# Kernel tuning notes

Hardware: AMD Instinct MI355X
Metric: run time of the kernel (lower is better)

Reference implementation:

```python
import jax, jax.numpy as jnp
import numpy as np

D_MODEL = 768
NUM_HEADS = 12
D_K = D_MODEL // NUM_HEADS


def setup_inputs() -> dict:
    key = jax.random.key(0)
    ks = jax.random.split(key, 9)
    B, S = 2, 4096
    x = jax.random.normal(ks[0], (B, S, D_MODEL), dtype=jnp.float32)
    s = 1.0 / np.sqrt(D_MODEL)
    Wq = jax.random.normal(ks[1], (D_MODEL, D_MODEL), dtype=jnp.float32) * s
    Wk = jax.random.normal(ks[2], (D_MODEL, D_MODEL), dtype=jnp.float32) * s
    Wv = jax.random.normal(ks[3], (D_MODEL, D_MODEL), dtype=jnp.float32) * s
    Wo = jax.random.normal(ks[4], (D_MODEL, D_MODEL), dtype=jnp.float32) * s
    bq = jnp.zeros((D_MODEL,), dtype=jnp.float32)
    bk = jnp.zeros((D_MODEL,), dtype=jnp.float32)
    bv = jnp.zeros((D_MODEL,), dtype=jnp.float32)
    bo = jnp.zeros((D_MODEL,), dtype=jnp.float32)
    return {"x": x, "Wq": Wq, "bq": bq, "Wk": Wk, "bk": bk,
            "Wv": Wv, "bv": bv, "Wo": Wo, "bo": bo}


def _split_heads(t):
    B, S, _ = t.shape
    return t.reshape(B, S, NUM_HEADS, D_K).transpose(0, 2, 1, 3)  # [B,H,S,d_k]


def reference(x, Wq, bq, Wk, bk, Wv, bv, Wo, bo):
    Q = _split_heads(x @ Wq.T + bq)
    K = _split_heads(x @ Wk.T + bk)
    V = _split_heads(x @ Wv.T + bv)
    scale = 1.0 / jnp.sqrt(jnp.float32(D_K))
    scores = jnp.einsum('bhqd,bhkd->bhqk', Q, K) * scale  # [B,H,S,S]
    attn = jax.nn.softmax(scores, axis=-1)
    out = jnp.einsum('bhqk,bhkd->bhqd', attn, V)          # [B,H,S,d_k]
    B, _, S, _ = out.shape
    out = out.transpose(0, 2, 1, 3).reshape(B, S, D_MODEL)
    return out @ Wo.T + bo
```

## Files before the change

kernel.cpp:

```cpp
#include <hip/hip_runtime.h>
#include <hip/hip_bf16.h>
#include <stdint.h>

typedef __hip_bfloat16 bf16;
typedef __attribute__((ext_vector_type(8))) short short8;
typedef __attribute__((ext_vector_type(4))) float f32x4;
typedef __attribute__((ext_vector_type(16))) float f32x16;

#define MFMA16(a, b, c) __builtin_amdgcn_mfma_f32_16x16x32_bf16((a), (b), (c), 0, 0, 0)
#define MFMA32(a, b, c) __builtin_amdgcn_mfma_f32_32x32x16_bf16((a), (b), (c), 0, 0, 0)

__device__ __forceinline__ unsigned short f2bf(float f) {
  bf16 h = __float2bfloat16(f);
  unsigned short u;
  __builtin_memcpy(&u, &h, 2);
  return u;
}

__device__ __forceinline__ uint32_t cvtpk(float lo, float hi) {
  uint32_t r;
  asm("v_cvt_pk_bf16_f32 %0, %1, %2" : "=v"(r) : "v"(lo), "v"(hi));
  return r;
}

__device__ __forceinline__ void pl32swap(uint32_t& a, uint32_t& b) {
  asm volatile("v_permlane32_swap_b32 %0, %1" : "+v"(a), "+v"(b));
}

__device__ __forceinline__ void gload_lds16(const void* g, void* l) {
  __builtin_amdgcn_global_load_lds(
      (const __attribute__((address_space(1))) uint32_t*)g,
      (__attribute__((address_space(3))) uint32_t*)l, 16, 0, 0);
}

__device__ __forceinline__ int swz_chunk(int row, int c) { return c ^ (row & 7); }

__global__ __launch_bounds__(256) void cvt_all(
    const float* __restrict__ x,
    const float* __restrict__ w0, const float* __restrict__ w1,
    const float* __restrict__ w2, const float* __restrict__ w3,
    bf16* __restrict__ xo,
    bf16* __restrict__ o0, bf16* __restrict__ o1,
    bf16* __restrict__ o2, bf16* __restrict__ o3) {
  int idx = blockIdx.x * 256 + threadIdx.x;
  const float* src;
  bf16* dst;
  int i;
  if (idx < 1572864) {
    src = x; dst = xo; i = idx;
  } else {
    int r = idx - 1572864;
    int w = r / 147456;
    i = r - w * 147456;
    src = (w == 0) ? w0 : (w == 1) ? w1 : (w == 2) ? w2 : w3;
    dst = (w == 0) ? o0 : (w == 1) ? o1 : (w == 2) ? o2 : o3;
  }
  float4 v = ((const float4*)src)[i];
  ushort4 u;
  u.x = f2bf(v.x); u.y = f2bf(v.y); u.z = f2bf(v.z); u.w = f2bf(v.w);
  ((ushort4*)dst)[i] = u;
}

__global__ __launch_bounds__(256, 4) void gemm_qkv(
    const bf16* __restrict__ A,
    const bf16* __restrict__ Wqb, const bf16* __restrict__ Wkb,
    const bf16* __restrict__ Wvb,
    const float* __restrict__ bq, const float* __restrict__ bk,
    const float* __restrict__ bv,
    bf16* __restrict__ Qh, bf16* __restrict__ Kh, bf16* __restrict__ Vh,
    float sq) {
  __shared__ bf16 As[128 * 64];
  __shared__ bf16 Bs[128 * 64];
  const int tid = threadIdx.x;
  const int lane = tid & 63, wid = tid >> 6;
  const int wr = wid >> 1, wc = wid & 1;
  const int l15 = lane & 15, lhi = lane >> 4;
  const int tm = blockIdx.x * 128;
  const int by = blockIdx.y;
  const int seg = by / 6;
  const int tn = (by - seg * 6) * 128;

  const bf16* B = (seg == 0) ? Wqb : (seg == 1) ? Wkb : Wvb;
  const float* bias = (seg == 0) ? bq : (seg == 1) ? bk : bv;
  bf16* dst = (seg == 0) ? Qh : (seg == 1) ? Kh : Vh;
  const float scale = (seg == 0) ? sq : 1.0f;
  const int K = 768;

  f32x4 zero = {0.f, 0.f, 0.f, 0.f};
  f32x4 acc[4][4];
  for (int i = 0; i < 4; ++i)
    for (int j = 0; j < 4; ++j) acc[i][j] = zero;

  for (int k0 = 0; k0 < K; k0 += 64) {
    __syncthreads();
    for (int it = 0; it < 4; ++it) {
      int o = (tid + it * 256) << 4;
      int row = o >> 7, c = (o >> 4) & 7;
      int sw = swz_chunk(row, c) << 4;
      gload_lds16((const char*)A + (((size_t)(tm + row) * K + k0) << 1) + sw, (char*)As + o);
      gload_lds16((const char*)B + (((size_t)(tn + row) * K + k0) << 1) + sw, (char*)Bs + o);
    }
    __syncthreads();
    for (int ks = 0; ks < 2; ++ks) {
      short8 af[4], bfr[4];
      for (int mi = 0; mi < 4; ++mi) {
        int row = wr * 64 + mi * 16 + l15;
        af[mi] = *(const short8*)((const char*)As + row * 128 +
                                  (swz_chunk(row, ks * 4 + lhi) << 4));
      }
      for (int ni = 0; ni < 4; ++ni) {
        int row = wc * 64 + ni * 16 + l15;
        bfr[ni] = *(const short8*)((const char*)Bs + row * 128 +
                                   (swz_chunk(row, ks * 4 + lhi) << 4));
      }
      for (int mi = 0; mi < 4; ++mi)
        for (int ni = 0; ni < 4; ++ni)
          acc[mi][ni] = MFMA16(af[mi], bfr[ni], acc[mi][ni]);
    }
  }

  for (int mi = 0; mi < 4; ++mi)
    for (int ni = 0; ni < 4; ++ni)
      for (int j = 0; j < 4; ++j) {
        int m = tm + wr * 64 + mi * 16 + lhi * 4 + j;
        int n = tn + wc * 64 + ni * 16 + l15;
        float v = (acc[mi][ni][j] + bias[n]) * scale;
        int b = m >> 12, s = m & 4095, h = n >> 6, d = n & 63;
        dst[(((size_t)(b * 12 + h) * 4096 + s) << 6) + d] = __float2bfloat16(v);
      }
}

__global__ __launch_bounds__(256, 4) void gemm_wo(
    const bf16* __restrict__ A, const bf16* __restrict__ B,
    const float* __restrict__ bias, float* __restrict__ C) {
  __shared__ bf16 As[128 * 64];
  __shared__ bf16 Bs[64 * 64];
  const int tid = threadIdx.x;
  const int lane = tid & 63, wid = tid >> 6;
  const int l15 = lane & 15, lhi = lane >> 4;
  const int tm = blockIdx.x * 128, tn = blockIdx.y * 64;
  const int K = 768;

  f32x4 zero = {0.f, 0.f, 0.f, 0.f};
  f32x4 acc[2][4];
  for (int i = 0; i < 2; ++i)
    for (int j = 0; j < 4; ++j) acc[i][j] = zero;

  for (int k0 = 0; k0 < K; k0 += 64) {
    __syncthreads();
    for (int it = 0; it < 4; ++it) {
      int o = (tid + it * 256) << 4;
      int row = o >> 7, c = (o >> 4) & 7;
      int sw = swz_chunk(row, c) << 4;
      gload_lds16((const char*)A + (((size_t)(tm + row) * K + k0) << 1) + sw, (char*)As + o);
    }
    for (int it = 0; it < 2; ++it) {
      int o = (tid + it * 256) << 4;
      int row = o >> 7, c = (o >> 4) & 7;
      int sw = swz_chunk(row, c) << 4;
      gload_lds16((const char*)B + (((size_t)(tn + row) * K + k0) << 1) + sw, (char*)Bs + o);
    }
    __syncthreads();
    for (int ks = 0; ks < 2; ++ks) {
      short8 af[2], bfr[4];
      for (int mi = 0; mi < 2; ++mi) {
        int row = wid * 32 + mi * 16 + l15;
        af[mi] = *(const short8*)((const char*)As + row * 128 +
                                  (swz_chunk(row, ks * 4 + lhi) << 4));
      }
      for (int ni = 0; ni < 4; ++ni) {
        int row = ni * 16 + l15;
        bfr[ni] = *(const short8*)((const char*)Bs + row * 128 +
                                   (swz_chunk(row, ks * 4 + lhi) << 4));
      }
      for (int mi = 0; mi < 2; ++mi)
        for (int ni = 0; ni < 4; ++ni)
          acc[mi][ni] = MFMA16(af[mi], bfr[ni], acc[mi][ni]);
    }
  }

  for (int mi = 0; mi < 2; ++mi)
    for (int ni = 0; ni < 4; ++ni)
      for (int j = 0; j < 4; ++j) {
        int m = tm + wid * 32 + mi * 16 + lhi * 4 + j;
        int n = tn + ni * 16 + l15;
        C[(size_t)m * 768 + n] = acc[mi][ni][j] + bias[n];
      }
}

__global__ __launch_bounds__(256) void transpose_v(const bf16* __restrict__ Vh,
                                                   bf16* __restrict__ VTh) {
  __shared__ bf16 T[64 * 64];
  const int tid = threadIdx.x;
  const int bh = blockIdx.x >> 6;
  const int t = blockIdx.x & 63;
  const char* src = (const char*)(Vh + ((size_t)bh * 4096 + t * 64) * 64);
  char* dst = (char*)(VTh + ((size_t)bh * 64) * 4096 + t * 64);

  for (int it = 0; it < 2; ++it) {
    int idx = tid + it * 256;
    int r = idx & 63, cc = idx >> 6;
    uint4 vv = *(const uint4*)(src + r * 128 + cc * 16);
    unsigned short sv[8];
    __builtin_memcpy(sv, &vv, 16);
#pragma unroll
    for (int jj = 0; jj < 8; ++jj) {
      int d = cc * 8 + jj;
      *(unsigned short*)((char*)T + d * 128 + (swz_chunk(d, r >> 3) << 4) +
                         ((r & 7) << 1)) = sv[jj];
    }
  }
  __syncthreads();
  for (int it = 0; it < 2; ++it) {
    int idx = tid + it * 256;
    int d = idx >> 3, c = idx & 7;
    uint4 vv = *(const uint4*)((const char*)T + d * 128 + (swz_chunk(d, c) << 4));
    *(uint4*)(dst + (size_t)d * 8192 + c * 16) = vv;
  }
}

__global__ __launch_bounds__(256, 3) void attn_kernel(
    const bf16* __restrict__ Qh, const bf16* __restrict__ Kh,
    const bf16* __restrict__ VTh, bf16* __restrict__ AO) {
  __shared__ float4 smem4[34816 / 16];
  char* smraw = (char*)smem4;
#define KT(b) (smraw + (b) * 8192)
#define VT(b) (smraw + 16384 + (b) * 8192)
  float* OX = (float*)smraw;

  const int tid = threadIdx.x;
  const int lane = tid & 63, wid = tid >> 6;
  const int l31 = lane & 31, h = lane >> 5;
  const int qsub = wid & 1, kvh = wid >> 1;

  const int bh = blockIdx.x >> 5;
  const int qt = blockIdx.x & 31;

  const size_t hb = (size_t)bh * 4096 * 64;
  const bf16* Qb = Qh + hb;
  const bf16* Kb = Kh + hb;
  const char* Vg0 = (const char*)(VTh + hb);
  const int qb = qt * 128 + qsub * 64;

  short8 qf[2][4];
#pragma unroll
  for (int j = 0; j < 2; ++j)
#pragma unroll
    for (int ki = 0; ki < 4; ++ki)
      qf[j][ki] = *(const short8*)((const char*)Qb + (size_t)(qb + 32 * j + l31) * 128 +
                                   ki * 32 + h * 16);

  f32x16 z16;
  for (int i = 0; i < 16; ++i) z16[i] = 0.f;
  f32x16 o00 = z16, o01 = z16, o10 = z16, o11 = z16;
  float psum0 = 0.f, psum1 = 0.f;

  const int krow = kvh * 32 + l31;

  for (int it = 0; it < 2; ++it) {
    int o = (tid + it * 256) << 4;
    int row = o >> 7, c = (o >> 4) & 7;
    int sw = swz_chunk(row, c) << 4;
    gload_lds16((const char*)Kb + row * 128 + sw, KT(0) + o);
    gload_lds16(Vg0 + row * 8192 + sw, VT(0) + o);
  }
  __syncthreads();

  int cur = 0;
  for (int kt = 0; kt < 64; ++kt) {
    if (kt < 63) {
      const char* Kg = (const char*)(Kb + (size_t)(kt + 1) * 4096);
      const char* Vg = Vg0 + (size_t)(kt + 1) * 128;
      char* Kd = KT(cur ^ 1);
      char* Vd = VT(cur ^ 1);
      for (int it = 0; it < 2; ++it) {
        int o = (tid + it * 256) << 4;
        int row = o >> 7, c = (o >> 4) & 7;
        int sw = swz_chunk(row, c) << 4;
        gload_lds16(Kg + row * 128 + sw, Kd + o);
        gload_lds16(Vg + row * 8192 + sw, Vd + o);
      }
    }

    const char* Kl = KT(cur);
    const char* Vl = VT(cur);

    f32x16 s0, s1;
    __builtin_amdgcn_s_setprio(1);
    {
      short8 kf = *(const short8*)(Kl + krow * 128 + (swz_chunk(krow, h) << 4));
      s0 = MFMA32(kf, qf[0][0], z16);
      s1 = MFMA32(kf, qf[1][0], z16);
    }
#pragma unroll
    for (int ki = 1; ki < 4; ++ki) {
      short8 kf = *(const short8*)(Kl + krow * 128 + (swz_chunk(krow, 2 * ki + h) << 4));
      s0 = MFMA32(kf, qf[0][ki], s0);
      s1 = MFMA32(kf, qf[1][ki], s1);
    }
    __builtin_amdgcn_s_setprio(0);

    short8 pb[2][2];
#pragma unroll
    for (int j = 0; j < 2; ++j) {
#pragma unroll
      for (int kk = 0; kk < 2; ++kk) {
        float p[8];
#pragma unroll
        for (int e = 0; e < 8; ++e)
          p[e] = __builtin_amdgcn_exp2f(j ? s1[8 * kk + e] : s0[8 * kk + e]);
        float ps = ((p[0] + p[1]) + (p[2] + p[3])) + ((p[4] + p[5]) + (p[6] + p[7]));
        if (j) psum1 += ps; else psum0 += ps;
        uint32_t A0 = cvtpk(p[0], p[1]), A1 = cvtpk(p[2], p[3]);
        uint32_t B0 = cvtpk(p[4], p[5]), B1 = cvtpk(p[6], p[7]);
        pl32swap(A0, B0);
        pl32swap(A1, B1);
        uint32_t w[4] = {A0, A1, B0, B1};
        short8 frag;
        __builtin_memcpy(&frag, w, 16);
        pb[j][kk] = frag;
      }
    }

    __builtin_amdgcn_s_setprio(1);
#pragma unroll
    for (int kk = 0; kk < 2; ++kk) {
      short8 v0 = *(const short8*)(Vl + l31 * 128 +
                                   (swz_chunk(l31, 4 * kvh + 2 * kk + h) << 4));
      short8 v1 = *(const short8*)(Vl + (32 + l31) * 128 +
                                   (swz_chunk(32 + l31, 4 * kvh + 2 * kk + h) << 4));
      o00 = MFMA32(v0, pb[0][kk], o00);
      o01 = MFMA32(v0, pb[1][kk], o01);
      o10 = MFMA32(v1, pb[0][kk], o10);
      o11 = MFMA32(v1, pb[1][kk], o11);
    }
    __builtin_amdgcn_s_setprio(0);

    __syncthreads();
    cur ^= 1;
  }

  psum0 += __shfl_xor(psum0, 32);
  psum1 += __shfl_xor(psum1, 32);

  float* W = OX + (size_t)(qsub * 64 + lane) * 68;
  if (kvh == 1) {
#pragma unroll
    for (int g = 0; g < 4; ++g) {
      *(float4*)(W + 0 * 16 + 4 * g) = make_float4(o00[4*g], o00[4*g+1], o00[4*g+2], o00[4*g+3]);
      *(float4*)(W + 1 * 16 + 4 * g) = make_float4(o01[4*g], o01[4*g+1], o01[4*g+2], o01[4*g+3]);
      *(float4*)(W + 2 * 16 + 4 * g) = make_float4(o10[4*g], o10[4*g+1], o10[4*g+2], o10[4*g+3]);
      *(float4*)(W + 3 * 16 + 4 * g) = make_float4(o11[4*g], o11[4*g+1], o11[4*g+2], o11[4*g+3]);
    }
    W[64] = psum0;
    W[65] = psum1;
  }
  __syncthreads();
  if (kvh == 0) {
#pragma unroll
    for (int g = 0; g < 4; ++g) {
      float4 a0 = *(const float4*)(W + 0 * 16 + 4 * g);
      float4 a1 = *(const float4*)(W + 1 * 16 + 4 * g);
      float4 a2 = *(const float4*)(W + 2 * 16 + 4 * g);
      float4 a3 = *(const float4*)(W + 3 * 16 + 4 * g);
      o00[4*g] += a0.x; o00[4*g+1] += a0.y; o00[4*g+2] += a0.z; o00[4*g+3] += a0.w;
      o01[4*g] += a1.x; o01[4*g+1] += a1.y; o01[4*g+2] += a1.z; o01[4*g+3] += a1.w;
      o10[4*g] += a2.x; o10[4*g+1] += a2.y; o10[4*g+2] += a2.z; o10[4*g+3] += a2.w;
      o11[4*g] += a3.x; o11[4*g+1] += a3.y; o11[4*g+2] += a3.z; o11[4*g+3] += a3.w;
    }
    psum0 += W[64];
    psum1 += W[65];
    float pinv0 = 1.0f / psum0;
    float pinv1 = 1.0f / psum1;

    const int b = bh / 12, hd = bh % 12;
#pragma unroll
    for (int j = 0; j < 2; ++j) {
      int q = qb + 32 * j + l31;
      char* base = (char*)AO + (((size_t)(b * 4096 + q)) * 768 + hd * 64) * 2;
      float pv = j ? pinv1 : pinv0;
#pragma unroll
      for (int t = 0; t < 2; ++t) {
#pragma unroll
        for (int u = 0; u < 4; ++u) {
          ushort4 us;
          float v0 = (t ? (j ? o11[4*u+0] : o10[4*u+0]) : (j ? o01[4*u+0] : o00[4*u+0]));
          float v1 = (t ? (j ? o11[4*u+1] : o10[4*u+1]) : (j ? o01[4*u+1] : o00[4*u+1]));
          float v2 = (t ? (j ? o11[4*u+2] : o10[4*u+2]) : (j ? o01[4*u+2] : o00[4*u+2]));
          float v3 = (t ? (j ? o11[4*u+3] : o10[4*u+3]) : (j ? o01[4*u+3] : o00[4*u+3]));
          us.x = f2bf(v0 * pv);
          us.y = f2bf(v1 * pv);
          us.z = f2bf(v2 * pv);
          us.w = f2bf(v3 * pv);
          int d0 = 32 * t + 8 * u + 4 * h;
          *(ushort4*)(base + d0 * 2) = us;
        }
      }
    }
  }
#undef KT
#undef VT
}

extern "C" void kernel_launch(void* const* d_in, const int* in_sizes, int n_in,
                              void* d_out, int out_size, void* d_ws, size_t ws_size,
                              hipStream_t stream) {
  (void)in_sizes; (void)n_in; (void)out_size; (void)ws_size;
  const float* x  = (const float*)d_in[0];
  const float* Wq = (const float*)d_in[1];
  const float* bq = (const float*)d_in[2];
  const float* Wk = (const float*)d_in[3];
  const float* bk = (const float*)d_in[4];
  const float* Wv = (const float*)d_in[5];
  const float* bv = (const float*)d_in[6];
  const float* Wo = (const float*)d_in[7];
  const float* bo = (const float*)d_in[8];

  char* ws = (char*)d_ws;
  bf16* Qh  = (bf16*)(ws + 0);
  bf16* Kh  = (bf16*)(ws + 12582912);
  bf16* Vh  = (bf16*)(ws + 25165824);
  bf16* xb  = (bf16*)(ws + 37748736);
  bf16* Wqb = (bf16*)(ws + 50331648);
  bf16* Wkb = (bf16*)(ws + 51511296);
  bf16* Wvb = (bf16*)(ws + 52690944);
  bf16* Wob = (bf16*)(ws + 53870592);
  bf16* VTh = xb;
  bf16* AO  = Vh;

  cvt_all<<<8448, 256, 0, stream>>>(x, Wq, Wk, Wv, Wo, xb, Wqb, Wkb, Wvb, Wob);

  const float SQ = 0.125f * 1.4426950408889634f;
  dim3 gq(64, 18);
  gemm_qkv<<<gq, 256, 0, stream>>>(xb, Wqb, Wkb, Wvb, bq, bk, bv,
                                   Qh, Kh, Vh, SQ);
  transpose_v<<<1536, 256, 0, stream>>>(Vh, VTh);
  attn_kernel<<<768, 256, 0, stream>>>(Qh, Kh, VTh, AO);
  dim3 gw(64, 12);
  gemm_wo<<<gw, 256, 0, stream>>>(AO, Wob, bo, (float*)d_out);
}
```

Baseline: 189.0 us.

## Software-pipeline attention loop: overlap next QK with previous PV, triple-buffer V

Restructures the attention main loop so each iteration computes QK^T for tile kt, then PV for tile kt-1 using probabilities from the prior iteration, then the exp for tile kt. This lets the MFMA work of the two matmuls interleave with the exp/convert work instead of running in strict dependency order. V gets a third LDS buffer, growing shared memory from about 34KB to 40KB, which may hurt occupancy at 3 blocks per CU. The V transpose kernel is also changed to pack two rows into 32-bit LDS writes with a simpler XOR swizzle, cutting LDS store count.

```diff
diff --git a/kernel.cpp b/kernel.cpp
--- a/kernel.cpp
+++ b/kernel.cpp
@@ -197,18 +197,17 @@
   const char* src = (const char*)(Vh + ((size_t)bh * 4096 + t * 64) * 64);
   char* dst = (char*)(VTh + ((size_t)bh * 64) * 4096 + t * 64);
 
-  for (int it = 0; it < 2; ++it) {
-    int idx = tid + it * 256;
-    int r = idx & 63, cc = idx >> 6;
-    uint4 vv = *(const uint4*)(src + r * 128 + cc * 16);
-    unsigned short sv[8];
-    __builtin_memcpy(sv, &vv, 16);
-#pragma unroll
-    for (int jj = 0; jj < 8; ++jj) {
-      int d = cc * 8 + jj;
-      *(unsigned short*)((char*)T + d * 128 + (swz_chunk(d, r >> 3) << 4) +
-                         ((r & 7) << 1)) = sv[jj];
-    }
+  const int rp = tid & 31, cc = tid >> 5;
+  uint4 va = *(const uint4*)(src + (2 * rp) * 128 + cc * 16);
+  uint4 vb = *(const uint4*)(src + (2 * rp + 1) * 128 + cc * 16);
+  unsigned short a16[8], b16[8];
+  __builtin_memcpy(a16, &va, 16);
+  __builtin_memcpy(b16, &vb, 16);
+#pragma unroll
+  for (int jj = 0; jj < 8; ++jj) {
+    uint32_t w = (uint32_t)a16[jj] | ((uint32_t)b16[jj] << 16);
+    *(uint32_t*)((char*)T + (cc * 8 + jj) * 128 + (((rp >> 2) ^ jj) << 4) +
+                 ((rp & 3) << 2)) = w;
   }
   __syncthreads();
   for (int it = 0; it < 2; ++it) {
@@ -222,10 +221,10 @@
 __global__ __launch_bounds__(256, 3) void attn_kernel(
     const bf16* __restrict__ Qh, const bf16* __restrict__ Kh,
     const bf16* __restrict__ VTh, bf16* __restrict__ AO) {
-  __shared__ float4 smem4[34816 / 16];
+  __shared__ float4 smem4[40960 / 16];
   char* smraw = (char*)smem4;
-#define KT(b) (smraw + (b) * 8192)
-#define VT(b) (smraw + 16384 + (b) * 8192)
+#define KTB(b) (smraw + (b) * 8192)
+#define VTB(b) (smraw + 16384 + (b) * 8192)
   float* OX = (float*)smraw;
 
   const int tid = threadIdx.x;
@@ -257,88 +256,99 @@
 
   const int krow = kvh * 32 + l31;
 
-  for (int it = 0; it < 2; ++it) {
-    int o = (tid + it * 256) << 4;
-    int row = o >> 7, c = (o >> 4) & 7;
-    int sw = swz_chunk(row, c) << 4;
-    gload_lds16((const char*)Kb + row * 128 + sw, KT(0) + o);
-    gload_lds16(Vg0 + row * 8192 + sw, VT(0) + o);
-  }
+#define STAGE_K(gbase, dstb)                                             \
+  for (int it = 0; it < 2; ++it) {                                       \
+    int o = (tid + it * 256) << 4;                                       \
+    int row = o >> 7, c = (o >> 4) & 7;                                  \
+    gload_lds16((gbase) + row * 128 + (swz_chunk(row, c) << 4), (dstb) + o); \
+  }
+#define STAGE_V(gbase, dstb)                                             \
+  for (int it = 0; it < 2; ++it) {                                       \
+    int o = (tid + it * 256) << 4;                                       \
+    int row = o >> 7, c = (o >> 4) & 7;                                  \
+    gload_lds16((gbase) + row * 8192 + (swz_chunk(row, c) << 4), (dstb) + o); \
+  }
+
+#define DO_QK(Kl)                                                        \
+  {                                                                      \
+    short8 kf = *(const short8*)((Kl) + krow * 128 + (swz_chunk(krow, h) << 4)); \
+    s0 = MFMA32(kf, qf[0][0], z16);                                      \
+    s1 = MFMA32(kf, qf[1][0], z16);                                      \
+  }                                                                      \
+  _Pragma("unroll")                                                      \
+  for (int ki = 1; ki < 4; ++ki) {                                       \
+    short8 kf = *(const short8*)((Kl) + krow * 128 + (swz_chunk(krow, 2 * ki + h) << 4)); \
+    s0 = MFMA32(kf, qf[0][ki], s0);                                      \
+    s1 = MFMA32(kf, qf[1][ki], s1);                                      \
+  }
+
+#define DO_PV(Vl)                                                        \
+  _Pragma("unroll")                                                      \
+  for (int kk = 0; kk < 2; ++kk) {                                       \
+    short8 v0 = *(const short8*)((Vl) + l31 * 128 +                      \
+                                 (swz_chunk(l31, 4 * kvh + 2 * kk + h) << 4)); \
+    short8 v1 = *(const short8*)((Vl) + (32 + l31) * 128 +               \
+                                 (swz_chunk(32 + l31, 4 * kvh + 2 * kk + h) << 4)); \
+    o00 = MFMA32(v0, pb[0][kk], o00);                                    \
+    o01 = MFMA32(v0, pb[1][kk], o01);                                    \
+    o10 = MFMA32(v1, pb[0][kk], o10);                                    \
+    o11 = MFMA32(v1, pb[1][kk], o11);                                    \
+  }
+
+#define DO_EXP()                                                         \
+  _Pragma("unroll")                                                      \
+  for (int j = 0; j < 2; ++j) {                                          \
+    _Pragma("unroll")                                                    \
+    for (int kk = 0; kk < 2; ++kk) {                                     \
+      float p[8];                                                        \
+      _Pragma("unroll")                                                  \
+      for (int e = 0; e < 8; ++e)                                        \
+        p[e] = __builtin_amdgcn_exp2f(j ? s1[8 * kk + e] : s0[8 * kk + e]); \
+      float ps = ((p[0] + p[1]) + (p[2] + p[3])) + ((p[4] + p[5]) + (p[6] + p[7])); \
+      if (j) psum1 += ps; else psum0 += ps;                              \
+      uint32_t A0 = cvtpk(p[0], p[1]), A1 = cvtpk(p[2], p[3]);           \
+      uint32_t B0 = cvtpk(p[4], p[5]), B1 = cvtpk(p[6], p[7]);           \
+      pl32swap(A0, B0);                                                  \
+      pl32swap(A1, B1);                                                  \
+      uint32_t w_[4] = {A0, A1, B0, B1};                                 \
+      short8 frag;                                                       \
+      __builtin_memcpy(&frag, w_, 16);                                   \
+      pb[j][kk] = frag;                                                  \
+    }                                                                    \
+  }
+
+  short8 pb[2][2];
+
+  STAGE_K((const char*)Kb, KTB(0));
+  STAGE_V(Vg0, VTB(0));
   __syncthreads();
-
-  int cur = 0;
-  for (int kt = 0; kt < 64; ++kt) {
+  STAGE_K((const char*)(Kb + (size_t)4096), KTB(1));
+  STAGE_V(Vg0 + (size_t)128, VTB(1));
+  {
+    f32x16 s0, s1;
+    DO_QK(KTB(0));
+    DO_EXP();
+  }
+
+  char* Vp = VTB(0);
+  char* Vc = VTB(1);
+  char* Vn = VTB(2);
+  for (int kt = 1; kt < 64; ++kt) {
+    __syncthreads();
     if (kt < 63) {
-      const char* Kg = (const char*)(Kb + (size_t)(kt + 1) * 4096);
-      const char* Vg = Vg0 + (size_t)(kt + 1) * 128;
-      char* Kd = KT(cur ^ 1);
-      char* Vd = VT(cur ^ 1);
-      for (int it = 0; it < 2; ++it) {
-        int o = (tid + it * 256) << 4;
-        int row = o >> 7, c = (o >> 4) & 7;
-        int sw = swz_chunk(row, c) << 4;
-        gload_lds16(Kg + row * 128 + sw, Kd + o);
-        gload_lds16(Vg + row * 8192 + sw, Vd + o);
-      }
-    }
-
-    const char* Kl = KT(cur);
-    const char* Vl = VT(cur);
-
+      STAGE_K((const char*)(Kb + (size_t)(kt + 1) * 4096), KTB((kt + 1) & 1));
+      STAGE_V(Vg0 + (size_t)(kt + 1) * 128, Vn);
+    }
     f32x16 s0, s1;
     __builtin_amdgcn_s_setprio(1);
-    {
-      short8 kf = *(const short8*)(Kl + krow * 128 + (swz_chunk(krow, h) << 4));
-      s0 = MFMA32(kf, qf[0][0], z16);
-      s1 = MFMA32(kf, qf[1][0], z16);
-    }
-#pragma unroll
-    for (int ki = 1; ki < 4; ++ki) {
-      short8 kf = *(const short8*)(Kl + krow * 128 + (swz_chunk(krow, 2 * ki + h) << 4));
-      s0 = MFMA32(kf, qf[0][ki], s0);
-      s1 = MFMA32(kf, qf[1][ki], s1);
-    }
+    DO_QK(KTB(kt & 1));
+    DO_PV(Vp);
     __builtin_amdgcn_s_setprio(0);
-
-    short8 pb[2][2];
-#pragma unroll
-    for (int j = 0; j < 2; ++j) {
-#pragma unroll
-      for (int kk = 0; kk < 2; ++kk) {
-        float p[8];
-#pragma unroll
-        for (int e = 0; e < 8; ++e)
-          p[e] = __builtin_amdgcn_exp2f(j ? s1[8 * kk + e] : s0[8 * kk + e]);
-        float ps = ((p[0] + p[1]) + (p[2] + p[3])) + ((p[4] + p[5]) + (p[6] + p[7]));
-        if (j) psum1 += ps; else psum0 += ps;
-        uint32_t A0 = cvtpk(p[0], p[1]), A1 = cvtpk(p[2], p[3]);
-        uint32_t B0 = cvtpk(p[4], p[5]), B1 = cvtpk(p[6], p[7]);
-        pl32swap(A0, B0);
-        pl32swap(A1, B1);
-        uint32_t w[4] = {A0, A1, B0, B1};
-        short8 frag;
-        __builtin_memcpy(&frag, w, 16);
-        pb[j][kk] = frag;
-      }
-    }
-
-    __builtin_amdgcn_s_setprio(1);
-#pragma unroll
-    for (int kk = 0; kk < 2; ++kk) {
-      short8 v0 = *(const short8*)(Vl + l31 * 128 +
-                                   (swz_chunk(l31, 4 * kvh + 2 * kk + h) << 4));
-      short8 v1 = *(const short8*)(Vl + (32 + l31) * 128 +
-                                   (swz_chunk(32 + l31, 4 * kvh + 2 * kk + h) << 4));
-      o00 = MFMA32(v0, pb[0][kk], o00);
-      o01 = MFMA32(v0, pb[1][kk], o01);
-      o10 = MFMA32(v1, pb[0][kk], o10);
-      o11 = MFMA32(v1, pb[1][kk], o11);
-    }
-    __builtin_amdgcn_s_setprio(0);
-
-    __syncthreads();
-    cur ^= 1;
-  }
+    DO_EXP();
+    char* t = Vp; Vp = Vc; Vc = Vn; Vn = t;
+  }
+  DO_PV(Vp);
+  __syncthreads();
 
   psum0 += __shfl_xor(psum0, 32);
   psum1 += __shfl_xor(psum1, 32);
@@ -398,8 +408,13 @@
       }
     }
   }
-#undef KT
-#undef VT
+#undef KTB
+#undef VTB
+#undef STAGE_K
+#undef STAGE_V
+#undef DO_QK
+#undef DO_PV
+#undef DO_EXP
 }
 
 extern "C" void kernel_launch(void* const* d_in, const int* in_sizes, int n_in,
```

Measured after the change: 294.5 us. 55.8% more time.
